# Optimization experiments

Measured on AMD Instinct MI355X. Metric: run time of the kernel, lower is better.

## Reference

```python
import jax, jax.numpy as jnp
import numpy as np

N = 2000
E = 20000
C = 16
B = 128
N_IN = 200   # first N_IN nodes are input nodes
N_OUT = 200  # last N_OUT nodes are output nodes
EPS = 1e-5


def setup_inputs() -> dict:
    key = jax.random.key(0)
    ks = jax.random.split(key, 8)
    x = jax.random.normal(ks[0], (B, N), dtype=jnp.float32)
    edge_index = jax.random.randint(ks[1], (2, E), 0, N, dtype=jnp.int32)
    input_node_mask = jnp.arange(N) < N_IN
    output_node_mask = jnp.arange(N) >= (N - N_OUT)
    func_mask = ~(input_node_mask | output_node_mask)
    # sparse-linear parameters (structured forms of W1/W2/W3)
    w1 = jax.random.normal(ks[2], (E, C), dtype=jnp.float32) * (1.0 / np.sqrt(C))
    b1 = jnp.zeros((N, C), dtype=jnp.float32)
    w2 = jax.random.normal(ks[3], (N, C, C), dtype=jnp.float32) * (1.0 / np.sqrt(C))
    b2 = jnp.zeros((N, C), dtype=jnp.float32)
    w3 = jax.random.normal(ks[4], (E, C), dtype=jnp.float32) * 1.0  # d=1 init scale
    b3 = jnp.zeros((E,), dtype=jnp.float32)
    g1 = jnp.ones((N * C,), dtype=jnp.float32)
    be1 = jnp.zeros((N * C,), dtype=jnp.float32)
    g2 = jnp.ones((N * C,), dtype=jnp.float32)
    be2 = jnp.zeros((N * C,), dtype=jnp.float32)
    return {"x": x, "w1": w1, "b1": b1, "w2": w2, "b2": b2, "w3": w3, "b3": b3,
            "g1": g1, "be1": be1, "g2": g2, "be2": be2,
            "edge_index": edge_index, "func_mask": func_mask,
            "output_node_mask": output_node_mask, "layers": 4}


def _batchnorm(h, g, b):
    # training-mode BatchNorm1d: batch mean and biased variance over axis 0
    m = h.mean(axis=0)
    v = h.var(axis=0)
    return (h - m) * jax.lax.rsqrt(v + EPS) * g + b


def reference(x, w1, b1, w2, b2, w3, b3, g1, be1, g2, be2,
              edge_index, func_mask, output_node_mask, layers):
    src, dst = edge_index[0], edge_index[1]
    Bsz, Nn = x.shape
    Ee, Cc = w1.shape
    fm = func_mask.astype(x.dtype)
    w2m = w2 * fm[:, None, None]          # W2 blocks exist only at function nodes
    w3m = w3 * fm[src][:, None]           # W3 rows exist only for edges with src in function nodes

    x0 = x[:, src]                        # node2edge: (B, E)
    xe = x0
    for _ in range(layers):
        # lin1: scatter edge values into dst node hidden channels
        contrib = xe.T[:, :, None] * w1[:, None, :]                    # (E, B, C)
        h = jax.ops.segment_sum(contrib, dst, num_segments=Nn)         # (N, B, C)
        h = jnp.transpose(h, (1, 0, 2)) + b1                           # (B, N, C)
        h = _batchnorm(h.reshape(Bsz, Nn * Cc), g1, be1)
        h = jax.nn.elu(h).reshape(Bsz, Nn, Cc)
        # lin2: block-diagonal C x C mix per (function) node
        h = jnp.einsum('bnc,ncd->bnd', h, w2m) + b2
        h = _batchnorm(h.reshape(Bsz, Nn * Cc), g2, be2)
        h = jax.nn.elu(h).reshape(Bsz, Nn, Cc)
        # lin3: gather src hidden, per-edge dot back to edge space
        xe = jnp.einsum('bec,ec->be', h[:, src], w3m) + b3             # (B, E)
        xe = xe + x0
    # edge2node: scatter-sum edge values to dst nodes, keep output nodes
    nodes = jax.ops.segment_sum(xe.T, dst, num_segments=Nn)            # (N, B)
    return nodes.T * output_node_mask.astype(x.dtype)
```

## Files before the change

kernel.cpp:

```cpp
#include <hip/hip_runtime.h>
#include <math.h>

#define BB 128
#define NN 2000
#define EE 20000
#define CC 16
#define FUNC_LO 200
#define FUNC_HI 1800
#define OUT_LO 1800
#define NFUNC 1600
#define EPSV 1e-5f
#define SS 40
#define HP 129

__global__ __launch_bounds__(256) void k_prep(
    const float* __restrict__ x, const int* __restrict__ ei,
    const float* __restrict__ w1, const float* __restrict__ w3,
    const float* __restrict__ b3,
    int* __restrict__ degIn, int* __restrict__ degOut,
    int* __restrict__ posIn,
    float* __restrict__ xT, float* __restrict__ w1s, float* __restrict__ w3s,
    float* __restrict__ b3s, int* __restrict__ inoff, int* __restrict__ wout,
    int* __restrict__ dstn, float* __restrict__ out)
{
    int t = blockIdx.x * 256 + threadIdx.x;
    if (t < EE) {
        int s = ei[t], d = ei[EE + t];
        int p = atomicAdd(&degIn[d], 1);
        int q = atomicAdd(&degOut[s], 1);
        int pi = d * SS + p, po = s * SS + q;
        posIn[t] = pi;
        inoff[pi] = s * BB;
        wout[po]  = pi * BB;
        dstn[po]  = d;
        b3s[po]   = b3[t];
        const float4* w1r = (const float4*)(w1 + (size_t)t * CC);
        float4*       w1d = (float4*)(w1s + (size_t)pi * CC);
        const float4* w3r = (const float4*)(w3 + (size_t)t * CC);
        float4*       w3d = (float4*)(w3s + (size_t)po * CC);
        #pragma unroll
        for (int i = 0; i < 4; i++) { w1d[i] = w1r[i]; w3d[i] = w3r[i]; }
    }
    if (t < NN * BB) {
        int b = t / NN, n = t - b * NN;
        xT[n * BB + b] = x[t];
        out[t] = 0.0f;
    }
}

__device__ __forceinline__ void bn_elu(float (&t)[CC],
                                       const float* __restrict__ g,
                                       const float* __restrict__ be,
                                       float* tile, float* part_s, float* part_ss,
                                       float* sc, float* sh, int b) {
    #pragma unroll
    for (int c = 0; c < CC; c++) tile[c * HP + b] = t[c];
    __syncthreads();
    {
        int c = b & 15, grp = b >> 4;
        float s = 0.f, ss = 0.f;
        #pragma unroll
        for (int i = 0; i < 16; i++) {
            float v = tile[c * HP + grp * 16 + i];
            s += v; ss += v * v;
        }
        part_s[grp * 16 + c] = s;
        part_ss[grp * 16 + c] = ss;
    }
    __syncthreads();
    if (b < CC) {
        float S = 0.f, SSm = 0.f;
        #pragma unroll
        for (int g8 = 0; g8 < 8; g8++) { S += part_s[g8 * 16 + b]; SSm += part_ss[g8 * 16 + b]; }
        float mean = S * (1.0f / BB);
        float var = SSm * (1.0f / BB) - mean * mean;
        float scale = rsqrtf(var + EPSV) * g[b];
        sc[b] = scale;
        sh[b] = be[b] - mean * scale;
    }
    __syncthreads();
    #pragma unroll
    for (int c = 0; c < CC; c++) {
        float u = t[c] * sc[c] + sh[c];
        t[c] = (u > 0.0f) ? u : (__expf(u) - 1.0f);
    }
}

__device__ __forceinline__ void fill_body(const int* __restrict__ ei,
    const int* __restrict__ posIn, const float* __restrict__ b3,
    const float* __restrict__ xT, float* __restrict__ xeA, float* __restrict__ xeB,
    float* __restrict__ out, int gtid, int gsize)
{
    for (int t = gtid; t < EE * BB; t += gsize) {
        int e = t >> 7, bb = t & 127;
        int s = ei[e];
        if (s >= FUNC_LO && s < FUNC_HI) continue;
        int d = ei[EE + e];
        float val = b3[e] + xT[s * BB + bb];
        if (d >= FUNC_LO && d < FUNC_HI) {
            int ro = posIn[e] * BB;
            xeA[ro + bb] = val;
            xeB[ro + bb] = val;
        } else if (d >= OUT_LO) {
            atomicAdd(&out[(size_t)bb * NN + d], val);
        }
    }
}

__global__ __launch_bounds__(128) void k_stage(
    const int* __restrict__ ei, const int* __restrict__ posIn,
    const float* __restrict__ b3,
    const float* __restrict__ xe_in, const int* __restrict__ inoff,
    const float* __restrict__ xT,
    const float* __restrict__ w1s, const float* __restrict__ w2,
    const float* __restrict__ w3s, const float* __restrict__ b3s,
    const int* __restrict__ wout, const int* __restrict__ dstn,
    const float* __restrict__ g1, const float* __restrict__ be1,
    const float* __restrict__ g2, const float* __restrict__ be2,
    const int* __restrict__ degIn, const int* __restrict__ degOut,
    float* __restrict__ xeA, float* __restrict__ xeB,
    float* __restrict__ xe_out, float* __restrict__ out, int lastFlag, int doFill)
{
    __shared__ float tile[CC * HP];
    __shared__ float part_s[128], part_ss[128];
    __shared__ float sc[CC], sh[CC];
    __shared__ float l_b3[SS];
    __shared__ int   l_dst[SS], l_wout[SS];

    const int b = threadIdx.x;
    const int n = FUNC_LO + blockIdx.x;
    const int base = n * SS;

    if (b < SS) {
        l_b3[b]   = b3s[base + b];
        l_dst[b]  = dstn[base + b];
        l_wout[b] = wout[base + b];
    }

    int dIn = degIn[n];
    int dOut = degOut[n];
    float x0r = xT[n * BB + b];

    if (doFill)
        fill_body(ei, posIn, b3, xT, xeA, xeB, out,
                  blockIdx.x * 128 + b, NFUNC * 128);

    float a[CC];
    #pragma unroll
    for (int c = 0; c < CC; c++) a[c] = 0.0f;

    for (int k0 = 0; k0 < dIn; k0 += 16) {
        float v[16];
        #pragma unroll
        for (int j = 0; j < 16; j++) {
            v[j] = 0.0f;
            if (k0 + j < dIn) {
                int ro = inoff ? inoff[base + k0 + j] : (base + k0 + j) * BB;
                v[j] = xe_in[ro + b];
            }
        }
        #pragma unroll
        for (int j = 0; j < 16; j++) {
            if (k0 + j < dIn) {
                const float* wr = &w1s[(size_t)(base + k0 + j) * CC];
                #pragma unroll
                for (int c = 0; c < CC; c++) a[c] += v[j] * wr[c];
            }
        }
    }

    bn_elu(a, g1 + n * CC, be1 + n * CC, tile, part_s, part_ss, sc, sh, b);

    float h2[CC];
    #pragma unroll
    for (int d = 0; d < CC; d++) h2[d] = 0.0f;
    const float* w2n = w2 + n * (CC * CC);
    #pragma unroll
    for (int c = 0; c < CC; c++) {
        float av = a[c];
        #pragma unroll
        for (int d = 0; d < CC; d++) h2[d] += av * w2n[c * CC + d];
    }

    bn_elu(h2, g2 + n * CC, be2 + n * CC, tile, part_s, part_ss, sc, sh, b);

    for (int q0 = 0; q0 < dOut; q0 += 4) {
        #pragma unroll
        for (int j = 0; j < 4; j++) {
            int q = q0 + j;
            if (q >= dOut) break;
            int dn = l_dst[q];
            bool live = lastFlag ? (dn >= OUT_LO) : (dn >= FUNC_LO && dn < FUNC_HI);
            if (!live) continue;
            const float* wr = &w3s[(size_t)(base + q) * CC];
            float val = l_b3[q] + x0r;
            #pragma unroll
            for (int d = 0; d < CC; d++) val += h2[d] * wr[d];
            if (lastFlag) atomicAdd(&out[(size_t)b * NN + dn], val);
            else          xe_out[l_wout[q] + b] = val;
        }
    }
}

extern "C" void kernel_launch(void* const* d_in, const int* in_sizes, int n_in,
                              void* d_out, int out_size, void* d_ws, size_t ws_size,
                              hipStream_t stream) {
    const float* x   = (const float*)d_in[0];
    const float* w1  = (const float*)d_in[1];
    const float* w2  = (const float*)d_in[3];
    const float* w3  = (const float*)d_in[5];
    const float* b3  = (const float*)d_in[6];
    const float* g1  = (const float*)d_in[7];
    const float* be1 = (const float*)d_in[8];
    const float* g2  = (const float*)d_in[9];
    const float* be2 = (const float*)d_in[10];
    const int* ei    = (const int*)d_in[11];
    float* out = (float*)d_out;

    char* ws = (char*)d_ws;
    float* xT   = (float*)ws;  ws += (size_t)NN * BB * 4;
    float* xeA  = (float*)ws;  ws += (size_t)NN * SS * BB * 4;
    float* xeB  = (float*)ws;  ws += (size_t)NN * SS * BB * 4;
    float* w1s  = (float*)ws;  ws += (size_t)NN * SS * CC * 4;
    float* w3s  = (float*)ws;  ws += (size_t)NN * SS * CC * 4;
    float* b3s  = (float*)ws;  ws += (size_t)NN * SS * 4;
    int* degIn  = (int*)ws;    ws += (size_t)NN * 4;
    int* degOut = (int*)ws;    ws += (size_t)NN * 4;
    int* posIn  = (int*)ws;    ws += (size_t)EE * 4;
    int* inoff  = (int*)ws;    ws += (size_t)NN * SS * 4;
    int* wout   = (int*)ws;    ws += (size_t)NN * SS * 4;
    int* dstn   = (int*)ws;    ws += (size_t)NN * SS * 4;

    hipMemsetAsync(degIn, 0, 2 * NN * sizeof(int), stream);
    k_prep<<<(NN * BB) / 256, 256, 0, stream>>>(x, ei, w1, w3, b3, degIn, degOut,
                                                posIn, xT, w1s, w3s, b3s,
                                                inoff, wout, dstn, out);

    const int* nullp = nullptr;
    k_stage<<<NFUNC, 128, 0, stream>>>(ei, posIn, b3, xT, inoff, xT, w1s, w2, w3s, b3s,
                                       wout, dstn, g1, be1, g2, be2, degIn, degOut,
                                       xeA, xeB, xeA, out, 0, 1);
    k_stage<<<NFUNC, 128, 0, stream>>>(ei, posIn, b3, xeA, nullp, xT, w1s, w2, w3s, b3s,
                                       wout, dstn, g1, be1, g2, be2, degIn, degOut,
                                       xeA, xeB, xeB, out, 0, 0);
    k_stage<<<NFUNC, 128, 0, stream>>>(ei, posIn, b3, xeB, nullp, xT, w1s, w2, w3s, b3s,
                                       wout, dstn, g1, be1, g2, be2, degIn, degOut,
                                       xeA, xeB, xeA, out, 0, 0);
    k_stage<<<NFUNC, 128, 0, stream>>>(ei, posIn, b3, xeA, nullp, xT, w1s, w2, w3s, b3s,
                                       wout, dstn, g1, be1, g2, be2, degIn, degOut,
                                       xeA, xeB, xeB, out, 1, 0);
}
```

Measured before the change: 175.6 us.

## Fuse prep and all layers into one persistent kernel with grid barriers

Replaces the prep kernel and four per-layer kernel launches with a single kernel of 1600 co-resident blocks that synchronise through a custom atomic-counter grid barrier with per-group flags. It also stages each node's w1/w3/w2 rows and index lists into LDS once for all four layers and reads them as float4. The aim is to remove launch gaps and repeated global weight loads. It depends on all 1600 blocks being resident at once (launch_bounds 128,4), otherwise the barrier deadlocks. The barrier's atomics and spinning add some latency at every phase.

```diff
diff --git a/kernel.cpp b/kernel.cpp
--- a/kernel.cpp
+++ b/kernel.cpp
@@ -12,40 +12,25 @@
 #define EPSV 1e-5f
 #define SS 40
 #define HP 129
-
-__global__ __launch_bounds__(256) void k_prep(
-    const float* __restrict__ x, const int* __restrict__ ei,
-    const float* __restrict__ w1, const float* __restrict__ w3,
-    const float* __restrict__ b3,
-    int* __restrict__ degIn, int* __restrict__ degOut,
-    int* __restrict__ posIn,
-    float* __restrict__ xT, float* __restrict__ w1s, float* __restrict__ w3s,
-    float* __restrict__ b3s, int* __restrict__ inoff, int* __restrict__ wout,
-    int* __restrict__ dstn, float* __restrict__ out)
-{
-    int t = blockIdx.x * 256 + threadIdx.x;
-    if (t < EE) {
-        int s = ei[t], d = ei[EE + t];
-        int p = atomicAdd(&degIn[d], 1);
-        int q = atomicAdd(&degOut[s], 1);
-        int pi = d * SS + p, po = s * SS + q;
-        posIn[t] = pi;
-        inoff[pi] = s * BB;
-        wout[po]  = pi * BB;
-        dstn[po]  = d;
-        b3s[po]   = b3[t];
-        const float4* w1r = (const float4*)(w1 + (size_t)t * CC);
-        float4*       w1d = (float4*)(w1s + (size_t)pi * CC);
-        const float4* w3r = (const float4*)(w3 + (size_t)t * CC);
-        float4*       w3d = (float4*)(w3s + (size_t)po * CC);
-        #pragma unroll
-        for (int i = 0; i < 4; i++) { w1d[i] = w1r[i]; w3d[i] = w3r[i]; }
-    }
-    if (t < NN * BB) {
-        int b = t / NN, n = t - b * NN;
-        xT[n * BB + b] = x[t];
-        out[t] = 0.0f;
-    }
+#define GSZ (NFUNC * 128)
+
+__device__ __forceinline__ void gbar(int* cnt, int* flags, int phase) {
+    __syncthreads();
+    if (threadIdx.x == 0) {
+        int old = __hip_atomic_fetch_add(cnt, 1, __ATOMIC_ACQ_REL, __HIP_MEMORY_SCOPE_AGENT);
+        if (old == phase * NFUNC - 1) {
+            #pragma unroll
+            for (int k = 0; k < 16; k++)
+                __hip_atomic_store(&flags[k * 16], phase, __ATOMIC_RELEASE,
+                                   __HIP_MEMORY_SCOPE_AGENT);
+        } else {
+            int* f = &flags[(blockIdx.x & 15) * 16];
+            while (__hip_atomic_load(f, __ATOMIC_RELAXED, __HIP_MEMORY_SCOPE_AGENT) < phase)
+                __builtin_amdgcn_s_sleep(8);
+            (void)__hip_atomic_load(f, __ATOMIC_ACQUIRE, __HIP_MEMORY_SCOPE_AGENT);
+        }
+    }
+    __syncthreads();
 }
 
 __device__ __forceinline__ void bn_elu(float (&t)[CC],
@@ -86,12 +71,141 @@
     }
 }
 
-__device__ __forceinline__ void fill_body(const int* __restrict__ ei,
-    const int* __restrict__ posIn, const float* __restrict__ b3,
-    const float* __restrict__ xT, float* __restrict__ xeA, float* __restrict__ xeB,
-    float* __restrict__ out, int gtid, int gsize)
+__device__ __forceinline__ void layer_lds(
+    const float* __restrict__ xe_in, const int* l_in ,
+    int dIn, int dOut, float x0r, int base,
+    const float* w1L, const float* w2L, const float* w3L,
+    const float* l_b3, const int* l_dst, const int* l_wout,
+    const float* __restrict__ g1n, const float* __restrict__ be1n,
+    const float* __restrict__ g2n, const float* __restrict__ be2n,
+    float* tile, float* part_s, float* part_ss, float* sc, float* sh,
+    float* __restrict__ xe_out, float* __restrict__ out, int lastFlag, int b)
 {
-    for (int t = gtid; t < EE * BB; t += gsize) {
+    float a[CC];
+    #pragma unroll
+    for (int c = 0; c < CC; c++) a[c] = 0.0f;
+
+    for (int k0 = 0; k0 < dIn; k0 += 16) {
+        float v[16];
+        #pragma unroll
+        for (int j = 0; j < 16; j++) {
+            v[j] = 0.0f;
+            if (k0 + j < dIn) {
+                int ro = l_in ? l_in[k0 + j] : (base + k0 + j) * BB;
+                v[j] = xe_in[ro + b];
+            }
+        }
+        #pragma unroll
+        for (int j = 0; j < 16; j++) {
+            if (k0 + j < dIn) {
+                const float4* wr = (const float4*)&w1L[(k0 + j) * CC];
+                float4 w0 = wr[0], w1_ = wr[1], w2_ = wr[2], w3_ = wr[3];
+                a[0] += v[j]*w0.x;  a[1] += v[j]*w0.y;  a[2] += v[j]*w0.z;  a[3] += v[j]*w0.w;
+                a[4] += v[j]*w1_.x; a[5] += v[j]*w1_.y; a[6] += v[j]*w1_.z; a[7] += v[j]*w1_.w;
+                a[8] += v[j]*w2_.x; a[9] += v[j]*w2_.y; a[10]+= v[j]*w2_.z; a[11]+= v[j]*w2_.w;
+                a[12]+= v[j]*w3_.x; a[13]+= v[j]*w3_.y; a[14]+= v[j]*w3_.z; a[15]+= v[j]*w3_.w;
+            }
+        }
+    }
+
+    bn_elu(a, g1n, be1n, tile, part_s, part_ss, sc, sh, b);
+
+    float h2[CC];
+    #pragma unroll
+    for (int d = 0; d < CC; d++) h2[d] = 0.0f;
+    #pragma unroll
+    for (int c = 0; c < CC; c++) {
+        float av = a[c];
+        const float4* wr = (const float4*)&w2L[c * CC];
+        float4 w0 = wr[0], w1_ = wr[1], w2_ = wr[2], w3_ = wr[3];
+        h2[0] += av*w0.x;  h2[1] += av*w0.y;  h2[2] += av*w0.z;  h2[3] += av*w0.w;
+        h2[4] += av*w1_.x; h2[5] += av*w1_.y; h2[6] += av*w1_.z; h2[7] += av*w1_.w;
+        h2[8] += av*w2_.x; h2[9] += av*w2_.y; h2[10]+= av*w2_.z; h2[11]+= av*w2_.w;
+        h2[12]+= av*w3_.x; h2[13]+= av*w3_.y; h2[14]+= av*w3_.z; h2[15]+= av*w3_.w;
+    }
+
+    bn_elu(h2, g2n, be2n, tile, part_s, part_ss, sc, sh, b);
+
+    for (int q = 0; q < dOut; q++) {
+        int dn = l_dst[q];
+        bool live = lastFlag ? (dn >= OUT_LO) : (dn >= FUNC_LO && dn < FUNC_HI);
+        if (!live) continue;
+        const float4* wr = (const float4*)&w3L[q * CC];
+        float4 w0 = wr[0], w1_ = wr[1], w2_ = wr[2], w3_ = wr[3];
+        float val = l_b3[q] + x0r;
+        val += h2[0]*w0.x + h2[1]*w0.y + h2[2]*w0.z + h2[3]*w0.w
+             + h2[4]*w1_.x + h2[5]*w1_.y + h2[6]*w1_.z + h2[7]*w1_.w
+             + h2[8]*w2_.x + h2[9]*w2_.y + h2[10]*w2_.z + h2[11]*w2_.w
+             + h2[12]*w3_.x + h2[13]*w3_.y + h2[14]*w3_.z + h2[15]*w3_.w;
+        if (lastFlag) atomicAdd(&out[(size_t)b * NN + dn], val);
+        else          xe_out[l_wout[q] + b] = val;
+    }
+}
+
+__global__ __launch_bounds__(128, 4) void k_mega(
+    const float* __restrict__ x, const int* __restrict__ ei,
+    const float* __restrict__ w1, const float* __restrict__ w3,
+    const float* __restrict__ b3, const float* __restrict__ w2,
+    const float* __restrict__ g1, const float* __restrict__ be1,
+    const float* __restrict__ g2, const float* __restrict__ be2,
+    float* __restrict__ xT, float* __restrict__ w1s, float* __restrict__ w3s,
+    float* __restrict__ b3s, int* __restrict__ posIn, int* __restrict__ inoff,
+    int* __restrict__ wout, int* __restrict__ dstn,
+    int* __restrict__ degIn, int* __restrict__ degOut,
+    int* cnt, int* flags,
+    float* __restrict__ xeA, float* __restrict__ xeB, float* __restrict__ out)
+{
+    const int tid = threadIdx.x;
+    const int blk = blockIdx.x;
+    const int gtid = blk * 128 + tid;
+    const int n = FUNC_LO + blk;
+    const int base = n * SS;
+
+    __shared__ float tile[CC * HP];
+    __shared__ float part_s[128], part_ss[128];
+    __shared__ float sc[CC], sh[CC];
+    __shared__ float w1L[SS * CC], w3L[SS * CC], w2L[CC * CC];
+    __shared__ float l_b3[SS];
+    __shared__ int   l_dst[SS], l_wout[SS], l_in[SS];
+
+    if (gtid < EE) {
+        int s = ei[gtid], d = ei[EE + gtid];
+        int p = atomicAdd(&degIn[d], 1);
+        int q = atomicAdd(&degOut[s], 1);
+        int pi = d * SS + p, po = s * SS + q;
+        posIn[gtid] = pi;
+        inoff[pi] = s * BB;
+        wout[po]  = pi * BB;
+        dstn[po]  = d;
+        b3s[po]   = b3[gtid];
+        const float4* w1r = (const float4*)(w1 + (size_t)gtid * CC);
+        float4*       w1d = (float4*)(w1s + (size_t)pi * CC);
+        const float4* w3r = (const float4*)(w3 + (size_t)gtid * CC);
+        float4*       w3d = (float4*)(w3s + (size_t)po * CC);
+        #pragma unroll
+        for (int i = 0; i < 4; i++) { w1d[i] = w1r[i]; w3d[i] = w3r[i]; }
+    }
+    for (int t = gtid; t < NN * BB; t += GSZ) {
+        int b2 = t / NN, n2 = t - b2 * NN;
+        xT[n2 * BB + b2] = x[t];
+        out[t] = 0.0f;
+    }
+
+    gbar(cnt, flags, 1);
+
+    for (int t = tid; t < SS * CC; t += 128) {
+        w1L[t] = w1s[(size_t)base * CC + t];
+        w3L[t] = w3s[(size_t)base * CC + t];
+    }
+    for (int t = tid; t < CC * CC; t += 128) w2L[t] = w2[(size_t)n * CC * CC + t];
+    if (tid < SS) {
+        l_b3[tid]  = b3s[base + tid];
+        l_dst[tid] = dstn[base + tid];
+        l_wout[tid]= wout[base + tid];
+        l_in[tid]  = inoff[base + tid];
+    }
+
+    for (int t = gtid; t < EE * BB; t += GSZ) {
         int e = t >> 7, bb = t & 127;
         int s = ei[e];
         if (s >= FUNC_LO && s < FUNC_HI) continue;
@@ -105,101 +219,27 @@
             atomicAdd(&out[(size_t)bb * NN + d], val);
         }
     }
-}
-
-__global__ __launch_bounds__(128) void k_stage(
-    const int* __restrict__ ei, const int* __restrict__ posIn,
-    const float* __restrict__ b3,
-    const float* __restrict__ xe_in, const int* __restrict__ inoff,
-    const float* __restrict__ xT,
-    const float* __restrict__ w1s, const float* __restrict__ w2,
-    const float* __restrict__ w3s, const float* __restrict__ b3s,
-    const int* __restrict__ wout, const int* __restrict__ dstn,
-    const float* __restrict__ g1, const float* __restrict__ be1,
-    const float* __restrict__ g2, const float* __restrict__ be2,
-    const int* __restrict__ degIn, const int* __restrict__ degOut,
-    float* __restrict__ xeA, float* __restrict__ xeB,
-    float* __restrict__ xe_out, float* __restrict__ out, int lastFlag, int doFill)
-{
-    __shared__ float tile[CC * HP];
-    __shared__ float part_s[128], part_ss[128];
-    __shared__ float sc[CC], sh[CC];
-    __shared__ float l_b3[SS];
-    __shared__ int   l_dst[SS], l_wout[SS];
-
-    const int b = threadIdx.x;
-    const int n = FUNC_LO + blockIdx.x;
-    const int base = n * SS;
-
-    if (b < SS) {
-        l_b3[b]   = b3s[base + b];
-        l_dst[b]  = dstn[base + b];
-        l_wout[b] = wout[base + b];
-    }
-
-    int dIn = degIn[n];
-    int dOut = degOut[n];
-    float x0r = xT[n * BB + b];
-
-    if (doFill)
-        fill_body(ei, posIn, b3, xT, xeA, xeB, out,
-                  blockIdx.x * 128 + b, NFUNC * 128);
-
-    float a[CC];
-    #pragma unroll
-    for (int c = 0; c < CC; c++) a[c] = 0.0f;
-
-    for (int k0 = 0; k0 < dIn; k0 += 16) {
-        float v[16];
-        #pragma unroll
-        for (int j = 0; j < 16; j++) {
-            v[j] = 0.0f;
-            if (k0 + j < dIn) {
-                int ro = inoff ? inoff[base + k0 + j] : (base + k0 + j) * BB;
-                v[j] = xe_in[ro + b];
-            }
-        }
-        #pragma unroll
-        for (int j = 0; j < 16; j++) {
-            if (k0 + j < dIn) {
-                const float* wr = &w1s[(size_t)(base + k0 + j) * CC];
-                #pragma unroll
-                for (int c = 0; c < CC; c++) a[c] += v[j] * wr[c];
-            }
-        }
-    }
-
-    bn_elu(a, g1 + n * CC, be1 + n * CC, tile, part_s, part_ss, sc, sh, b);
-
-    float h2[CC];
-    #pragma unroll
-    for (int d = 0; d < CC; d++) h2[d] = 0.0f;
-    const float* w2n = w2 + n * (CC * CC);
-    #pragma unroll
-    for (int c = 0; c < CC; c++) {
-        float av = a[c];
-        #pragma unroll
-        for (int d = 0; d < CC; d++) h2[d] += av * w2n[c * CC + d];
-    }
-
-    bn_elu(h2, g2 + n * CC, be2 + n * CC, tile, part_s, part_ss, sc, sh, b);
-
-    for (int q0 = 0; q0 < dOut; q0 += 4) {
-        #pragma unroll
-        for (int j = 0; j < 4; j++) {
-            int q = q0 + j;
-            if (q >= dOut) break;
-            int dn = l_dst[q];
-            bool live = lastFlag ? (dn >= OUT_LO) : (dn >= FUNC_LO && dn < FUNC_HI);
-            if (!live) continue;
-            const float* wr = &w3s[(size_t)(base + q) * CC];
-            float val = l_b3[q] + x0r;
-            #pragma unroll
-            for (int d = 0; d < CC; d++) val += h2[d] * wr[d];
-            if (lastFlag) atomicAdd(&out[(size_t)b * NN + dn], val);
-            else          xe_out[l_wout[q] + b] = val;
-        }
-    }
+    __syncthreads();
+
+    const int dIn  = degIn[n];
+    const int dOut = degOut[n];
+    const float x0r = xT[n * BB + tid];
+
+    layer_lds(xT, l_in, dIn, dOut, x0r, base, w1L, w2L, w3L, l_b3, l_dst, l_wout,
+              g1 + n*CC, be1 + n*CC, g2 + n*CC, be2 + n*CC,
+              tile, part_s, part_ss, sc, sh, xeA, out, 0, tid);
+    gbar(cnt, flags, 2);
+    layer_lds(xeA, nullptr, dIn, dOut, x0r, base, w1L, w2L, w3L, l_b3, l_dst, l_wout,
+              g1 + n*CC, be1 + n*CC, g2 + n*CC, be2 + n*CC,
+              tile, part_s, part_ss, sc, sh, xeB, out, 0, tid);
+    gbar(cnt, flags, 3);
+    layer_lds(xeB, nullptr, dIn, dOut, x0r, base, w1L, w2L, w3L, l_b3, l_dst, l_wout,
+              g1 + n*CC, be1 + n*CC, g2 + n*CC, be2 + n*CC,
+              tile, part_s, part_ss, sc, sh, xeA, out, 0, tid);
+    gbar(cnt, flags, 4);
+    layer_lds(xeA, nullptr, dIn, dOut, x0r, base, w1L, w2L, w3L, l_b3, l_dst, l_wout,
+              g1 + n*CC, be1 + n*CC, g2 + n*CC, be2 + n*CC,
+              tile, part_s, part_ss, sc, sh, xeB, out, 1, tid);
 }
 
 extern "C" void kernel_launch(void* const* d_in, const int* in_sizes, int n_in,
@@ -224,29 +264,18 @@
     float* w1s  = (float*)ws;  ws += (size_t)NN * SS * CC * 4;
     float* w3s  = (float*)ws;  ws += (size_t)NN * SS * CC * 4;
     float* b3s  = (float*)ws;  ws += (size_t)NN * SS * 4;
-    int* degIn  = (int*)ws;    ws += (size_t)NN * 4;
-    int* degOut = (int*)ws;    ws += (size_t)NN * 4;
     int* posIn  = (int*)ws;    ws += (size_t)EE * 4;
     int* inoff  = (int*)ws;    ws += (size_t)NN * SS * 4;
     int* wout   = (int*)ws;    ws += (size_t)NN * SS * 4;
     int* dstn   = (int*)ws;    ws += (size_t)NN * SS * 4;
-
-    hipMemsetAsync(degIn, 0, 2 * NN * sizeof(int), stream);
-    k_prep<<<(NN * BB) / 256, 256, 0, stream>>>(x, ei, w1, w3, b3, degIn, degOut,
-                                                posIn, xT, w1s, w3s, b3s,
-                                                inoff, wout, dstn, out);
-
-    const int* nullp = nullptr;
-    k_stage<<<NFUNC, 128, 0, stream>>>(ei, posIn, b3, xT, inoff, xT, w1s, w2, w3s, b3s,
-                                       wout, dstn, g1, be1, g2, be2, degIn, degOut,
-                                       xeA, xeB, xeA, out, 0, 1);
-    k_stage<<<NFUNC, 128, 0, stream>>>(ei, posIn, b3, xeA, nullp, xT, w1s, w2, w3s, b3s,
-                                       wout, dstn, g1, be1, g2, be2, degIn, degOut,
-                                       xeA, xeB, xeB, out, 0, 0);
-    k_stage<<<NFUNC, 128, 0, stream>>>(ei, posIn, b3, xeB, nullp, xT, w1s, w2, w3s, b3s,
-                                       wout, dstn, g1, be1, g2, be2, degIn, degOut,
-                                       xeA, xeB, xeA, out, 0, 0);
-    k_stage<<<NFUNC, 128, 0, stream>>>(ei, posIn, b3, xeA, nullp, xT, w1s, w2, w3s, b3s,
-                                       wout, dstn, g1, be1, g2, be2, degIn, degOut,
-                                       xeA, xeB, xeB, out, 1, 0);
-}
+    int* degIn  = (int*)ws;    ws += (size_t)NN * 4;
+    int* degOut = (int*)ws;    ws += (size_t)NN * 4;
+    int* cnt    = (int*)ws;    ws += 4;
+    ws += 12;
+    int* flags  = (int*)ws;    ws += 256 * 4;
+
+    hipMemsetAsync(degIn, 0, (2 * NN + 4 + 256) * sizeof(int), stream);
+    k_mega<<<NFUNC, 128, 0, stream>>>(x, ei, w1, w3, b3, w2, g1, be1, g2, be2,
+                                      xT, w1s, w3s, b3s, posIn, inoff, wout, dstn,
+                                      degIn, degOut, cnt, flags, xeA, xeB, out);
+}
```

New measurement: 420.1 us. 139% more time.

## Split edge-fill into its own kernel and slim the per-layer kernel

Applied to the files above, without the earlier changes.

Moves the input-edge fill, which seeds xeA/xeB and the output atomics for non-function-source edges, out of the first layer kernel into a separate one-block-per-edge kernel. The layer kernel loses the fill loop, the shared-memory staging of b3/dst/wout (now read straight from global), and its gather unroll drops from 16 to 8. This is meant to lower register and shared-memory pressure and remove the grid-stride fill from the critical first layer. The cost is an extra launch of 20000 mostly early-exiting blocks and uncached global reads in the output loop.

```diff
diff --git a/kernel.cpp b/kernel.cpp
--- a/kernel.cpp
+++ b/kernel.cpp
@@ -48,6 +48,26 @@
     }
 }
 
+__global__ __launch_bounds__(128) void k_fill(
+    const int* __restrict__ ei, const int* __restrict__ posIn,
+    const float* __restrict__ b3, const float* __restrict__ xT,
+    float* __restrict__ xeA, float* __restrict__ xeB, float* __restrict__ out)
+{
+    int e = blockIdx.x;
+    int s = ei[e];
+    if (s >= FUNC_LO && s < FUNC_HI) return;
+    int d = ei[EE + e];
+    int b = threadIdx.x;
+    float val = b3[e] + xT[s * BB + b];
+    if (d >= FUNC_LO && d < FUNC_HI) {
+        int ro = posIn[e] * BB;
+        xeA[ro + b] = val;
+        xeB[ro + b] = val;
+    } else if (d >= OUT_LO) {
+        atomicAdd(&out[(size_t)b * NN + d], val);
+    }
+}
+
 __device__ __forceinline__ void bn_elu(float (&t)[CC],
                                        const float* __restrict__ g,
                                        const float* __restrict__ be,
@@ -86,30 +106,7 @@
     }
 }
 
-__device__ __forceinline__ void fill_body(const int* __restrict__ ei,
-    const int* __restrict__ posIn, const float* __restrict__ b3,
-    const float* __restrict__ xT, float* __restrict__ xeA, float* __restrict__ xeB,
-    float* __restrict__ out, int gtid, int gsize)
-{
-    for (int t = gtid; t < EE * BB; t += gsize) {
-        int e = t >> 7, bb = t & 127;
-        int s = ei[e];
-        if (s >= FUNC_LO && s < FUNC_HI) continue;
-        int d = ei[EE + e];
-        float val = b3[e] + xT[s * BB + bb];
-        if (d >= FUNC_LO && d < FUNC_HI) {
-            int ro = posIn[e] * BB;
-            xeA[ro + bb] = val;
-            xeB[ro + bb] = val;
-        } else if (d >= OUT_LO) {
-            atomicAdd(&out[(size_t)bb * NN + d], val);
-        }
-    }
-}
-
-__global__ __launch_bounds__(128) void k_stage(
-    const int* __restrict__ ei, const int* __restrict__ posIn,
-    const float* __restrict__ b3,
+__global__ __launch_bounds__(128) void k_layer(
     const float* __restrict__ xe_in, const int* __restrict__ inoff,
     const float* __restrict__ xT,
     const float* __restrict__ w1s, const float* __restrict__ w2,
@@ -118,41 +115,28 @@
     const float* __restrict__ g1, const float* __restrict__ be1,
     const float* __restrict__ g2, const float* __restrict__ be2,
     const int* __restrict__ degIn, const int* __restrict__ degOut,
-    float* __restrict__ xeA, float* __restrict__ xeB,
-    float* __restrict__ xe_out, float* __restrict__ out, int lastFlag, int doFill)
+    float* __restrict__ xe_out, float* __restrict__ out, int lastFlag)
 {
+    const int b = threadIdx.x;
+    const int n = FUNC_LO + blockIdx.x;
+    const int base = n * SS;
+
     __shared__ float tile[CC * HP];
     __shared__ float part_s[128], part_ss[128];
     __shared__ float sc[CC], sh[CC];
-    __shared__ float l_b3[SS];
-    __shared__ int   l_dst[SS], l_wout[SS];
-
-    const int b = threadIdx.x;
-    const int n = FUNC_LO + blockIdx.x;
-    const int base = n * SS;
-
-    if (b < SS) {
-        l_b3[b]   = b3s[base + b];
-        l_dst[b]  = dstn[base + b];
-        l_wout[b] = wout[base + b];
-    }
 
     int dIn = degIn[n];
     int dOut = degOut[n];
     float x0r = xT[n * BB + b];
 
-    if (doFill)
-        fill_body(ei, posIn, b3, xT, xeA, xeB, out,
-                  blockIdx.x * 128 + b, NFUNC * 128);
-
     float a[CC];
     #pragma unroll
     for (int c = 0; c < CC; c++) a[c] = 0.0f;
 
-    for (int k0 = 0; k0 < dIn; k0 += 16) {
-        float v[16];
-        #pragma unroll
-        for (int j = 0; j < 16; j++) {
+    for (int k0 = 0; k0 < dIn; k0 += 8) {
+        float v[8];
+        #pragma unroll
+        for (int j = 0; j < 8; j++) {
             v[j] = 0.0f;
             if (k0 + j < dIn) {
                 int ro = inoff ? inoff[base + k0 + j] : (base + k0 + j) * BB;
@@ -160,7 +144,7 @@
             }
         }
         #pragma unroll
-        for (int j = 0; j < 16; j++) {
+        for (int j = 0; j < 8; j++) {
             if (k0 + j < dIn) {
                 const float* wr = &w1s[(size_t)(base + k0 + j) * CC];
                 #pragma unroll
@@ -189,15 +173,16 @@
         for (int j = 0; j < 4; j++) {
             int q = q0 + j;
             if (q >= dOut) break;
-            int dn = l_dst[q];
+            int sl = base + q;
+            int dn = dstn[sl];
             bool live = lastFlag ? (dn >= OUT_LO) : (dn >= FUNC_LO && dn < FUNC_HI);
             if (!live) continue;
-            const float* wr = &w3s[(size_t)(base + q) * CC];
-            float val = l_b3[q] + x0r;
+            const float* wr = &w3s[(size_t)sl * CC];
+            float val = b3s[sl] + x0r;
             #pragma unroll
             for (int d = 0; d < CC; d++) val += h2[d] * wr[d];
             if (lastFlag) atomicAdd(&out[(size_t)b * NN + dn], val);
-            else          xe_out[l_wout[q] + b] = val;
+            else          xe_out[wout[sl] + b] = val;
         }
     }
 }
@@ -235,18 +220,15 @@
     k_prep<<<(NN * BB) / 256, 256, 0, stream>>>(x, ei, w1, w3, b3, degIn, degOut,
                                                 posIn, xT, w1s, w3s, b3s,
                                                 inoff, wout, dstn, out);
+    k_fill<<<EE, 128, 0, stream>>>(ei, posIn, b3, xT, xeA, xeB, out);
 
     const int* nullp = nullptr;
-    k_stage<<<NFUNC, 128, 0, stream>>>(ei, posIn, b3, xT, inoff, xT, w1s, w2, w3s, b3s,
-                                       wout, dstn, g1, be1, g2, be2, degIn, degOut,
-                                       xeA, xeB, xeA, out, 0, 1);
-    k_stage<<<NFUNC, 128, 0, stream>>>(ei, posIn, b3, xeA, nullp, xT, w1s, w2, w3s, b3s,
-                                       wout, dstn, g1, be1, g2, be2, degIn, degOut,
-                                       xeA, xeB, xeB, out, 0, 0);
-    k_stage<<<NFUNC, 128, 0, stream>>>(ei, posIn, b3, xeB, nullp, xT, w1s, w2, w3s, b3s,
-                                       wout, dstn, g1, be1, g2, be2, degIn, degOut,
-                                       xeA, xeB, xeA, out, 0, 0);
-    k_stage<<<NFUNC, 128, 0, stream>>>(ei, posIn, b3, xeA, nullp, xT, w1s, w2, w3s, b3s,
-                                       wout, dstn, g1, be1, g2, be2, degIn, degOut,
-                                       xeA, xeB, xeB, out, 1, 0);
-}
+    k_layer<<<NFUNC, 128, 0, stream>>>(xT,  inoff, xT, w1s, w2, w3s, b3s, wout, dstn,
+                                       g1, be1, g2, be2, degIn, degOut, xeA, out, 0);
+    k_layer<<<NFUNC, 128, 0, stream>>>(xeA, nullp, xT, w1s, w2, w3s, b3s, wout, dstn,
+                                       g1, be1, g2, be2, degIn, degOut, xeB, out, 0);
+    k_layer<<<NFUNC, 128, 0, stream>>>(xeB, nullp, xT, w1s, w2, w3s, b3s, wout, dstn,
+                                       g1, be1, g2, be2, degIn, degOut, xeA, out, 0);
+    k_layer<<<NFUNC, 128, 0, stream>>>(xeA, nullp, xT, w1s, w2, w3s, b3s, wout, dstn,
+                                       g1, be1, g2, be2, degIn, degOut, xeB, out, 1);
+}
```

Result: slower. 181.6 us (+3.4%).
